# Kernel tuning notes

Measured on AMD Instinct MI355X. Metric: run time of the kernel, lower is better.

Reference implementation:

```python
import jax, jax.numpy as jnp
import numpy as np

B, T, M, PH, PW = 4, 8, 128, 48, 48
QD, CD, H, DH = 1024, 768, 8, 64
INNER = H * DH

def layer_norm(x, g, b, eps=1e-5):
    m = x.mean(-1, keepdims=True)
    v = ((x - m) ** 2).mean(-1, keepdims=True)
    return (x - m) * jax.lax.rsqrt(v + eps) * g + b

def setup_inputs():
    key = jax.random.key(0)
    ks = jax.random.split(key, 10)
    x = jax.random.normal(ks[0], (B * T, PH * PW, QD), jnp.float32)
    context = jax.random.normal(ks[1], (B, M, CD), jnp.float32)
    sg_node_positions = jax.random.normal(ks[2], (B, M, 3), jnp.float32) * 2.0
    # valid c2w: identity rotation + random translation (invertible)
    c2w = jnp.broadcast_to(jnp.eye(4, dtype=jnp.float32), (B, T, 4, 4))
    camera_c2w = c2w.at[..., :3, 3].set(jax.random.normal(ks[3], (B, T, 3), jnp.float32))
    intrinsics = jnp.broadcast_to(jnp.array([[1.0, 0.0, 0.5], [0.0, 1.0, 0.5], [0.0, 0.0, 1.0]], jnp.float32), (B, 3, 3))
    s = 0.02
    Wq = jax.random.normal(ks[4], (QD, INNER), jnp.float32) * s
    Wk = jax.random.normal(ks[5], (CD, INNER), jnp.float32) * s
    Wv = jax.random.normal(ks[6], (CD, INNER), jnp.float32) * s
    Wo = jax.random.normal(ks[7], (INNER, QD), jnp.float32) * s
    gate = jnp.array([0.1], jnp.float32)          # zero-init in module; nonzero so path is active
    spatial_gate = jnp.array([0.1], jnp.float32)
    spatial_log_sigma = jax.random.normal(ks[8], (H,), jnp.float32) * 0.1
    depth_log_alpha = jax.random.normal(ks[9], (H,), jnp.float32) * 0.1
    gamma_q = jnp.ones((QD,), jnp.float32); beta_q = jnp.zeros((QD,), jnp.float32)
    gamma_k = jnp.ones((CD,), jnp.float32); beta_k = jnp.zeros((CD,), jnp.float32)
    return dict(x=x, context=context, sg_node_positions=sg_node_positions, camera_c2w=camera_c2w,
                intrinsics=intrinsics, Wq=Wq, Wk=Wk, Wv=Wv, Wo=Wo, gate=gate, spatial_gate=spatial_gate,
                spatial_log_sigma=spatial_log_sigma, depth_log_alpha=depth_log_alpha,
                gamma_q=gamma_q, beta_q=beta_q, gamma_k=gamma_k, beta_k=beta_k,
                patch_h=PH, patch_w=PW)

def spatial_bias(sg_node_positions, camera_c2w, intrinsics, spatial_log_sigma, depth_log_alpha, patch_h, patch_w):
    Bb, Mn, _ = sg_node_positions.shape
    Tn = camera_c2w.shape[1]
    w2c = jnp.linalg.inv(camera_c2w)
    R = w2c[:, :, :3, :3]
    tv = w2c[:, :, :3, 3]
    p_cam = jnp.einsum('btij,bmj->btmi', R, sg_node_positions) + tv[:, :, None, :]  # (B,T,M,3)
    z = jnp.clip(p_cam[..., 2], 1e-4, None)
    fx = intrinsics[:, 0, 0]; fy = intrinsics[:, 1, 1]
    cx = intrinsics[:, 0, 2]; cy = intrinsics[:, 1, 2]
    u = fx[:, None, None] * (p_cam[..., 0] / z) + cx[:, None, None]   # (B,T,M)
    v = fy[:, None, None] * (p_cam[..., 1] / z) + cy[:, None, None]
    gy = (jnp.arange(patch_h, dtype=jnp.float32) + 0.5) / patch_h
    gx = (jnp.arange(patch_w, dtype=jnp.float32) + 0.5) / patch_w
    gyy, gxx = jnp.meshgrid(gy, gx, indexing='ij')
    gxx = gxx.reshape(-1); gyy = gyy.reshape(-1)                       # (P,)
    sq = (gxx[None, None, :, None] - u[:, :, None, :]) ** 2 + (gyy[None, None, :, None] - v[:, :, None, :]) ** 2  # (B,T,P,M)
    sigma = jnp.exp(spatial_log_sigma)
    inv2s = z[:, :, None, :] ** 2 / (2.0 * sigma[None, None, :, None] ** 2 + 1e-8)  # (B,T,H,M)
    bias = -sq[:, :, None, :, :] * inv2s[:, :, :, None, :]             # (B,T,H,P,M)
    depth_term = depth_log_alpha[None, None, :, None, None] * (-jnp.log(z))[:, :, None, None, :]
    bias = bias + depth_term
    behind = p_cam[..., 2] <= 0.0
    bias = jnp.where(behind[:, :, None, None, :], 0.0, bias)
    return bias.reshape(Bb * Tn, bias.shape[2], patch_h * patch_w, Mn)  # (BT,H,P,M)

def reference(x, context, sg_node_positions, camera_c2w, intrinsics, Wq, Wk, Wv, Wo, gate, spatial_gate,
              spatial_log_sigma, depth_log_alpha, gamma_q, beta_q, gamma_k, beta_k, patch_h, patch_w):
    BT, P, _ = x.shape
    Bb, Mn, _ = context.shape
    Tn = camera_c2w.shape[1]
    q = layer_norm(x, gamma_q, beta_q) @ Wq                            # (BT,P,INNER)
    ck = layer_norm(context, gamma_k, beta_k)
    k = ck @ Wk
    v = ck @ Wv
    q = q.reshape(BT, P, H, DH).transpose(0, 2, 1, 3)                  # (BT,H,P,DH)
    k = jnp.broadcast_to(k.reshape(Bb, 1, Mn, H, DH), (Bb, Tn, Mn, H, DH)).reshape(BT, Mn, H, DH).transpose(0, 2, 1, 3)
    v = jnp.broadcast_to(v.reshape(Bb, 1, Mn, H, DH), (Bb, Tn, Mn, H, DH)).reshape(BT, Mn, H, DH).transpose(0, 2, 1, 3)
    scores = jnp.einsum('bhpd,bhmd->bhpm', q, k) * (DH ** -0.5)        # (BT,H,P,M)
    bias = spatial_bias(sg_node_positions, camera_c2w, intrinsics, spatial_log_sigma, depth_log_alpha, patch_h, patch_w)
    scores = scores + jnp.tanh(spatial_gate) * bias
    attn = jax.nn.softmax(scores, axis=-1)
    out = jnp.einsum('bhpm,bhmd->bhpd', attn, v).transpose(0, 2, 1, 3).reshape(BT, P, INNER)
    return x + jnp.tanh(gate) * (out @ Wo)
```

## Files before the change

### kernel.cpp

```cpp
#include <hip/hip_runtime.h>
#include <hip/hip_bf16.h>
#include <stdint.h>
#include <cstddef>

typedef short short8 __attribute__((ext_vector_type(8)));
typedef float f32x4 __attribute__((ext_vector_type(4)));
typedef unsigned short us4 __attribute__((ext_vector_type(4)));

#define DEV static __device__ __forceinline__

DEV unsigned short f2b(float f) {
  __hip_bfloat16 h = __float2bfloat16(f);
  return __builtin_bit_cast(unsigned short, h);
}

DEV void gload_lds16(const void* g, void* lds) {
  __builtin_amdgcn_global_load_lds((const __attribute__((address_space(1))) unsigned int*)g,
                                   (__attribute__((address_space(3))) unsigned int*)lds, 16, 0, 0);
}

template<int EPI>
__launch_bounds__(256, 2)
__global__ void gemm_bt(const unsigned short* __restrict__ A,
                        const unsigned short* __restrict__ Bt,
                        unsigned short* __restrict__ Cb,
                        float* __restrict__ Cf,
                        const float* __restrict__ xres,
                        const float* __restrict__ gatep,
                        int M, int N, int K)
{
  __shared__ __attribute__((aligned(16))) char As[16384];
  __shared__ __attribute__((aligned(16))) char Bs[16384];
  const int tid  = threadIdx.x;
  const int lane = tid & 63, w = tid >> 6;
  const int wr = w >> 1, wc = w & 1;
  const int g = lane >> 4, lr = lane & 15;
  const int ntile = N >> 7;
  const int m0 = (blockIdx.x / ntile) << 7;
  const int n0 = (blockIdx.x % ntile) << 7;

  const int lrow  = lane >> 3;
  const int lslot = (lane & 7) ^ lrow;

  f32x4 acc[4][4] = {};

  for (int k0 = 0; k0 < K; k0 += 64) {
#pragma unroll
    for (int c = 0; c < 4; ++c) {
      const int rowc = (w*4 + c)*8;
      gload_lds16(A  + (size_t)(m0 + rowc + lrow)*K + k0 + lslot*8, As + rowc*128);
      gload_lds16(Bt + (size_t)(n0 + rowc + lrow)*K + k0 + lslot*8, Bs + rowc*128);
    }
    __syncthreads();
#pragma unroll
    for (int ks = 0; ks < 2; ++ks) {
      short8 af[4], bfr[4];
#pragma unroll
      for (int mt = 0; mt < 4; ++mt) {
        int row = wr*64 + mt*16 + lr;
        int slot = (ks*4 + g) ^ (row & 7);
        af[mt] = *(const short8*)(As + row*128 + slot*16);
      }
#pragma unroll
      for (int nt = 0; nt < 4; ++nt) {
        int row = wc*64 + nt*16 + lr;
        int slot = (ks*4 + g) ^ (row & 7);
        bfr[nt] = *(const short8*)(Bs + row*128 + slot*16);
      }
#pragma unroll
      for (int mt = 0; mt < 4; ++mt)
#pragma unroll
        for (int nt = 0; nt < 4; ++nt)
          acc[mt][nt] = __builtin_amdgcn_mfma_f32_16x16x32_bf16(af[mt], bfr[nt], acc[mt][nt], 0, 0, 0);
    }
    __syncthreads();
  }

  if (EPI == 1) {
    const float tg = tanhf(gatep[0]);
#pragma unroll
    for (int mt = 0; mt < 4; ++mt)
#pragma unroll
      for (int nt = 0; nt < 4; ++nt)
#pragma unroll
        for (int r = 0; r < 4; ++r) {
          size_t row = (size_t)(m0 + wr*64 + mt*16 + g*4 + r);
          size_t col = (size_t)(n0 + wc*64 + nt*16 + lr);
          size_t idx = row * (size_t)N + col;
          Cf[idx] = xres[idx] + tg * acc[mt][nt][r];
        }
  } else {
#pragma unroll
    for (int mt = 0; mt < 4; ++mt)
#pragma unroll
      for (int nt = 0; nt < 4; ++nt)
#pragma unroll
        for (int r = 0; r < 4; ++r) {
          size_t row = (size_t)(m0 + wr*64 + mt*16 + g*4 + r);
          size_t col = (size_t)(n0 + wc*64 + nt*16 + lr);
          Cb[row * (size_t)N + col] = f2b(acc[mt][nt][r]);
        }
  }
}

template<int NSEG>
__global__ void ln_rows(const float* __restrict__ in, const float* __restrict__ gamma,
                        const float* __restrict__ beta, unsigned short* __restrict__ out, int C)
{
  const int lane = threadIdx.x & 63;
  const size_t row = (size_t)blockIdx.x*4 + (threadIdx.x >> 6);
  const float* rp = in + row * (size_t)C;
  f32x4 vals[NSEG];
  float s = 0.f, sq = 0.f;
#pragma unroll
  for (int i = 0; i < NSEG; ++i) {
    f32x4 v = *(const f32x4*)(rp + (i*64 + lane)*4);
    vals[i] = v;
#pragma unroll
    for (int j = 0; j < 4; ++j) { s += v[j]; sq += v[j]*v[j]; }
  }
#pragma unroll
  for (int off = 32; off >= 1; off >>= 1) {
    s  += __shfl_xor(s, off);
    sq += __shfl_xor(sq, off);
  }
  const float invC = 1.0f / (float)C;
  float mean = s * invC;
  float var  = sq * invC - mean*mean;
  float rstd = rsqrtf(var + 1e-5f);
#pragma unroll
  for (int i = 0; i < NSEG; ++i) {
    int cb = (i*64 + lane)*4;
    f32x4 gm = *(const f32x4*)(gamma + cb);
    f32x4 bb = *(const f32x4*)(beta + cb);
    us4 ov;
#pragma unroll
    for (int j = 0; j < 4; ++j)
      ov[j] = f2b((vals[i][j] - mean)*rstd*gm[j] + bb[j]);
    *(us4*)(out + row * (size_t)C + cb) = ov;
  }
}

__global__ void transpose_cast(const float* __restrict__ src, unsigned short* __restrict__ dst,
                               int R, int C)
{
  __shared__ float tile[32][33];
  const int cb = C >> 5;
  const int bx = blockIdx.x % cb, by = blockIdx.x / cb;
  const int tx = threadIdx.x & 31, ty = threadIdx.x >> 5;
#pragma unroll
  for (int i = 0; i < 32; i += 8)
    tile[ty + i][tx] = src[(size_t)(by*32 + ty + i)*C + bx*32 + tx];
  __syncthreads();
#pragma unroll
  for (int i = 0; i < 32; i += 8)
    dst[(size_t)(bx*32 + ty + i)*R + by*32 + tx] = f2b(tile[tx][ty + i]);
}

__global__ void spatial_pre(const float* __restrict__ pos, const float* __restrict__ c2w,
                            const float* __restrict__ intr, const float* __restrict__ sls,
                            const float* __restrict__ dla,
                            float* __restrict__ u_o, float* __restrict__ v_o, float* __restrict__ bh_o,
                            float* __restrict__ iv_o, float* __restrict__ dp_o)
{
  const int bt = blockIdx.x;
  const int b = bt >> 3;
  const int m = threadIdx.x;
  const float* Mc = c2w + (size_t)bt*16;
  float r00=Mc[0], r01=Mc[1], r02=Mc[2],  t0=Mc[3];
  float r10=Mc[4], r11=Mc[5], r12=Mc[6],  t1=Mc[7];
  float r20=Mc[8], r21=Mc[9], r22=Mc[10], t2=Mc[11];
  float a00 = r11*r22 - r12*r21;
  float a01 = r02*r21 - r01*r22;
  float a02 = r01*r12 - r02*r11;
  float a10 = r12*r20 - r10*r22;
  float a11 = r00*r22 - r02*r20;
  float a12 = r02*r10 - r00*r12;
  float a20 = r10*r21 - r11*r20;
  float a21 = r01*r20 - r00*r21;
  float a22 = r00*r11 - r01*r10;
  float det = r00*a00 + r01*a10 + r02*a20;
  float id = 1.0f/det;
  a00*=id; a01*=id; a02*=id; a10*=id; a11*=id; a12*=id; a20*=id; a21*=id; a22*=id;
  float tv0 = -(a00*t0 + a01*t1 + a02*t2);
  float tv1 = -(a10*t0 + a11*t1 + a12*t2);
  float tv2 = -(a20*t0 + a21*t1 + a22*t2);
  const float* pm = pos + (size_t)(b*128 + m)*3;
  float px = pm[0], py = pm[1], pz = pm[2];
  float x = a00*px + a01*py + a02*pz + tv0;
  float y = a10*px + a11*py + a12*pz + tv1;
  float zraw = a20*px + a21*py + a22*pz + tv2;
  float z = fmaxf(zraw, 1e-4f);
  float fx = intr[b*9 + 0], fy = intr[b*9 + 4], cx = intr[b*9 + 2], cy = intr[b*9 + 5];
  u_o[bt*128 + m] = fx*(x/z) + cx;
  v_o[bt*128 + m] = fy*(y/z) + cy;
  bh_o[bt*128 + m] = (zraw <= 0.0f) ? 1.0f : 0.0f;
  float lz = __logf(z);
#pragma unroll
  for (int hh = 0; hh < 8; ++hh) {
    float sg = __expf(sls[hh]);
    iv_o[(size_t)(bt*8 + hh)*128 + m] = z*z / (2.0f*sg*sg + 1e-8f);
    dp_o[(size_t)(bt*8 + hh)*128 + m] = dla[hh] * (-lz);
  }
}

__global__ void reshuffle_kv(const unsigned short* __restrict__ kproj,
                             const unsigned short* __restrict__ vproj,
                             unsigned short* __restrict__ Kb, unsigned short* __restrict__ Vt)
{
  int idx = blockIdx.x*256 + threadIdx.x;
  int d  = idx & 63;
  int hh = (idx >> 6) & 7;
  int m  = (idx >> 9) & 127;
  int b  = idx >> 16;
  unsigned short kv = kproj[idx];
  unsigned short vv = vproj[idx];
  Kb[(((size_t)(b*8 + hh))*128 + m)*64 + d] = kv;
  Vt[(((size_t)(b*8 + hh))*64 + d)*128 + m] = vv;
}

__launch_bounds__(256, 2)
__global__ void attn_kernel(const unsigned short* __restrict__ q,
                            const unsigned short* __restrict__ Kb,
                            const unsigned short* __restrict__ Vt,
                            const float* __restrict__ ub, const float* __restrict__ vb,
                            const float* __restrict__ bhb,
                            const float* __restrict__ ivb, const float* __restrict__ dpb,
                            const float* __restrict__ sgate,
                            unsigned short* __restrict__ out)
{
  const int bid = blockIdx.x;
  const int ptile = bid % 18;
  const int h  = (bid / 18) & 7;
  const int bt = bid / (18*8);
  const int b  = bt >> 3;
  const int lane = threadIdx.x & 63, w = threadIdx.x >> 6;
  const int g = lane >> 4, lr = lane & 15;
  const int p0 = ptile*128 + w*32;

  const float sg = tanhf(sgate[0]);
  const unsigned short* Kh = Kb + ((size_t)(b*8 + h)) * (128*64);
  const unsigned short* Vh = Vt + ((size_t)(b*8 + h)) * (64*128);
  const unsigned short* qh = q + (size_t)bt*2304*512 + h*64;

  short8 qf[2][2];
#pragma unroll
  for (int pt = 0; pt < 2; ++pt)
#pragma unroll
    for (int ks = 0; ks < 2; ++ks)
      qf[pt][ks] = *(const short8*)(qh + (size_t)(p0 + pt*16 + lr)*512 + ks*32 + g*8);

  f32x4 st[8][2] = {};
#pragma unroll
  for (int mt = 0; mt < 8; ++mt) {
#pragma unroll
    for (int ks = 0; ks < 2; ++ks) {
      short8 kf = *(const short8*)(Kh + (mt*16 + lr)*64 + ks*32 + g*8);
#pragma unroll
      for (int pt = 0; pt < 2; ++pt)
        st[mt][pt] = __builtin_amdgcn_mfma_f32_16x16x32_bf16(kf, qf[pt][ks], st[mt][pt], 0, 0, 0);
    }
  }

  float gx[2], gy[2];
#pragma unroll
  for (int pt = 0; pt < 2; ++pt) {
    int p = p0 + pt*16 + lr;
    int py = p / 48, px = p - py*48;
    gx[pt] = (px + 0.5f) * (1.0f/48.0f);
    gy[pt] = (py + 0.5f) * (1.0f/48.0f);
  }
  const float* uB = ub  + bt*128;
  const float* vB = vb  + bt*128;
  const float* bB = bhb + bt*128;
  const float* iB = ivb + (size_t)(bt*8 + h)*128;
  const float* dB = dpb + (size_t)(bt*8 + h)*128;

  float pmax[2] = {-3.0e38f, -3.0e38f};
#pragma unroll
  for (int mt = 0; mt < 8; ++mt) {
    int mb = mt*16 + g*4;
    f32x4 uu = *(const f32x4*)(uB + mb);
    f32x4 vv = *(const f32x4*)(vB + mb);
    f32x4 bh = *(const f32x4*)(bB + mb);
    f32x4 iv = *(const f32x4*)(iB + mb);
    f32x4 dp = *(const f32x4*)(dB + mb);
#pragma unroll
    for (int r = 0; r < 4; ++r) {
#pragma unroll
      for (int pt = 0; pt < 2; ++pt) {
        float du = gx[pt] - uu[r], dv = gy[pt] - vv[r];
        float bias = (bh[r] != 0.0f) ? 0.0f : (-(du*du + dv*dv)*iv[r] + dp[r]);
        float s = st[mt][pt][r]*0.125f + sg*bias;
        st[mt][pt][r] = s;
        pmax[pt] = fmaxf(pmax[pt], s);
      }
    }
  }
#pragma unroll
  for (int pt = 0; pt < 2; ++pt) {
    pmax[pt] = fmaxf(pmax[pt], __shfl_xor(pmax[pt], 16));
    pmax[pt] = fmaxf(pmax[pt], __shfl_xor(pmax[pt], 32));
  }
  float psum[2] = {0.f, 0.f};
#pragma unroll
  for (int mt = 0; mt < 8; ++mt)
#pragma unroll
    for (int pt = 0; pt < 2; ++pt)
#pragma unroll
      for (int r = 0; r < 4; ++r) {
        float e = __expf(st[mt][pt][r] - pmax[pt]);
        st[mt][pt][r] = e;
        psum[pt] += e;
      }
#pragma unroll
  for (int pt = 0; pt < 2; ++pt) {
    psum[pt] += __shfl_xor(psum[pt], 16);
    psum[pt] += __shfl_xor(psum[pt], 32);
  }
  float pinv[2] = {1.0f/psum[0], 1.0f/psum[1]};

  short8 pf[2][4];
#pragma unroll
  for (int pt = 0; pt < 2; ++pt)
#pragma unroll
    for (int ms = 0; ms < 4; ++ms)
#pragma unroll
      for (int i = 0; i < 8; ++i)
        pf[pt][ms][i] = (short)f2b(st[ms*2 + (i>>2)][pt][i & 3] * pinv[pt]);

  f32x4 o[4][2] = {};
#pragma unroll
  for (int ms = 0; ms < 4; ++ms) {
#pragma unroll
    for (int dt = 0; dt < 4; ++dt) {
      const unsigned short* vp = Vh + (size_t)(dt*16 + lr)*128 + ms*32 + g*4;
      us4 v0 = *(const us4*)(vp);
      us4 v1 = *(const us4*)(vp + 16);
      short8 vf;
#pragma unroll
      for (int i = 0; i < 4; ++i) { vf[i] = (short)v0[i]; vf[i+4] = (short)v1[i]; }
#pragma unroll
      for (int pt = 0; pt < 2; ++pt)
        o[dt][pt] = __builtin_amdgcn_mfma_f32_16x16x32_bf16(vf, pf[pt][ms], o[dt][pt], 0, 0, 0);
    }
  }

#pragma unroll
  for (int dt = 0; dt < 4; ++dt)
#pragma unroll
    for (int pt = 0; pt < 2; ++pt) {
      int p = p0 + pt*16 + lr;
      int d = h*64 + dt*16 + g*4;
      us4 ov;
#pragma unroll
      for (int r = 0; r < 4; ++r) ov[r] = f2b(o[dt][pt][r]);
      *(us4*)(out + (size_t)(bt*2304 + p)*512 + d) = ov;
    }
}

extern "C" void kernel_launch(void* const* d_in, const int* in_sizes, int n_in,
                              void* d_out, int out_size, void* d_ws, size_t ws_size,
                              hipStream_t stream)
{
  const float* x     = (const float*)d_in[0];
  const float* ctx   = (const float*)d_in[1];
  const float* pos   = (const float*)d_in[2];
  const float* c2w   = (const float*)d_in[3];
  const float* intr  = (const float*)d_in[4];
  const float* Wq    = (const float*)d_in[5];
  const float* Wk    = (const float*)d_in[6];
  const float* Wv    = (const float*)d_in[7];
  const float* Wo    = (const float*)d_in[8];
  const float* gate  = (const float*)d_in[9];
  const float* sgate = (const float*)d_in[10];
  const float* sls   = (const float*)d_in[11];
  const float* dla   = (const float*)d_in[12];
  const float* gq    = (const float*)d_in[13];
  const float* bq    = (const float*)d_in[14];
  const float* gk    = (const float*)d_in[15];
  const float* bk    = (const float*)d_in[16];

  char* ws = (char*)d_ws;
  size_t off = 0;
  auto alloc = [&](size_t bytes) {
    char* p = ws + off;
    off += (bytes + 255) & ~(size_t)255;
    return p;
  };
  unsigned short* ln_x  = (unsigned short*)alloc(73728ull*1024*2);
  unsigned short* qbuf  = (unsigned short*)alloc(73728ull*512*2);
  unsigned short* Wq_t  = (unsigned short*)alloc(512ull*1024*2);
  unsigned short* Wk_t  = (unsigned short*)alloc(512ull*768*2);
  unsigned short* Wv_t  = (unsigned short*)alloc(512ull*768*2);
  unsigned short* Wo_t  = (unsigned short*)alloc(1024ull*512*2);
  unsigned short* ck    = (unsigned short*)alloc(512ull*768*2);
  unsigned short* kproj = (unsigned short*)alloc(512ull*512*2);
  unsigned short* vproj = (unsigned short*)alloc(512ull*512*2);
  unsigned short* Kbuf  = (unsigned short*)alloc(4ull*8*128*64*2);
  unsigned short* Vtb   = (unsigned short*)alloc(4ull*8*64*128*2);
  float* u_o  = (float*)alloc(32*128*4);
  float* v_o  = (float*)alloc(32*128*4);
  float* bh_o = (float*)alloc(32*128*4);
  float* iv_o = (float*)alloc(32ull*8*128*4);
  float* dp_o = (float*)alloc(32ull*8*128*4);
  unsigned short* attn_out = ln_x;

  transpose_cast<<<(512/32)*(1024/32), 256, 0, stream>>>(Wq, Wq_t, 1024, 512);
  transpose_cast<<<(512/32)*(768/32),  256, 0, stream>>>(Wk, Wk_t, 768, 512);
  transpose_cast<<<(512/32)*(768/32),  256, 0, stream>>>(Wv, Wv_t, 768, 512);
  transpose_cast<<<(1024/32)*(512/32), 256, 0, stream>>>(Wo, Wo_t, 512, 1024);

  ln_rows<4><<<73728/4, 256, 0, stream>>>(x, gq, bq, ln_x, 1024);
  ln_rows<3><<<512/4,   256, 0, stream>>>(ctx, gk, bk, ck, 768);

  spatial_pre<<<32, 128, 0, stream>>>(pos, c2w, intr, sls, dla, u_o, v_o, bh_o, iv_o, dp_o);

  gemm_bt<0><<<(512/128)*(512/128), 256, 0, stream>>>(ck, Wk_t, kproj, nullptr, nullptr, nullptr, 512, 512, 768);
  gemm_bt<0><<<(512/128)*(512/128), 256, 0, stream>>>(ck, Wv_t, vproj, nullptr, nullptr, nullptr, 512, 512, 768);
  reshuffle_kv<<<262144/256, 256, 0, stream>>>(kproj, vproj, Kbuf, Vtb);

  gemm_bt<0><<<(73728/128)*(512/128), 256, 0, stream>>>(ln_x, Wq_t, qbuf, nullptr, nullptr, nullptr, 73728, 512, 1024);

  attn_kernel<<<32*8*18, 256, 0, stream>>>(qbuf, Kbuf, Vtb, u_o, v_o, bh_o, iv_o, dp_o, sgate, attn_out);

  gemm_bt<1><<<(73728/128)*(1024/128), 256, 0, stream>>>(attn_out, Wo_t, nullptr, (float*)d_out, x, gate, 73728, 1024, 512);
}
```

Before: 559.8 us.

## Fuse attention with output projection and KV GEMMs with reshuffle

The attention kernel now handles all 8 heads for a 64-row patch tile, keeps the attention output in LDS, and runs the Wo projection plus the gated residual epilogue in the same kernel. This removes the bf16 attention-output round trip through global memory. The K/V projections are merged into one kernel that writes the head-major layout directly, which drops the reshuffle kernel, and the four weight transposes become one launch. In exchange, the fused kernel uses 80KB of LDS and launches only 1152 blocks, so occupancy drops, and each block reloads the full Wo matrix.

```diff
diff --git a/kernel.cpp b/kernel.cpp
--- a/kernel.cpp
+++ b/kernel.cpp
@@ -19,14 +19,10 @@
                                    (__attribute__((address_space(3))) unsigned int*)lds, 16, 0, 0);
 }
 
-template<int EPI>
 __launch_bounds__(256, 2)
 __global__ void gemm_bt(const unsigned short* __restrict__ A,
                         const unsigned short* __restrict__ Bt,
                         unsigned short* __restrict__ Cb,
-                        float* __restrict__ Cf,
-                        const float* __restrict__ xres,
-                        const float* __restrict__ gatep,
                         int M, int N, int K)
 {
   __shared__ __attribute__((aligned(16))) char As[16384];
@@ -76,31 +72,86 @@
     __syncthreads();
   }
 
-  if (EPI == 1) {
-    const float tg = tanhf(gatep[0]);
-#pragma unroll
-    for (int mt = 0; mt < 4; ++mt)
-#pragma unroll
-      for (int nt = 0; nt < 4; ++nt)
-#pragma unroll
-        for (int r = 0; r < 4; ++r) {
-          size_t row = (size_t)(m0 + wr*64 + mt*16 + g*4 + r);
-          size_t col = (size_t)(n0 + wc*64 + nt*16 + lr);
-          size_t idx = row * (size_t)N + col;
-          Cf[idx] = xres[idx] + tg * acc[mt][nt][r];
-        }
-  } else {
-#pragma unroll
-    for (int mt = 0; mt < 4; ++mt)
-#pragma unroll
-      for (int nt = 0; nt < 4; ++nt)
-#pragma unroll
-        for (int r = 0; r < 4; ++r) {
-          size_t row = (size_t)(m0 + wr*64 + mt*16 + g*4 + r);
-          size_t col = (size_t)(n0 + wc*64 + nt*16 + lr);
-          Cb[row * (size_t)N + col] = f2b(acc[mt][nt][r]);
-        }
-  }
+#pragma unroll
+  for (int mt = 0; mt < 4; ++mt)
+#pragma unroll
+    for (int nt = 0; nt < 4; ++nt)
+#pragma unroll
+      for (int r = 0; r < 4; ++r) {
+        size_t row = (size_t)(m0 + wr*64 + mt*16 + g*4 + r);
+        size_t col = (size_t)(n0 + wc*64 + nt*16 + lr);
+        Cb[row * (size_t)N + col] = f2b(acc[mt][nt][r]);
+      }
+}
+
+__launch_bounds__(256, 2)
+__global__ void gemm_kv(const unsigned short* __restrict__ ck,
+                        const unsigned short* __restrict__ Wk_t,
+                        const unsigned short* __restrict__ Wv_t,
+                        unsigned short* __restrict__ Kb,
+                        unsigned short* __restrict__ Vt)
+{
+  __shared__ __attribute__((aligned(16))) char As[16384];
+  __shared__ __attribute__((aligned(16))) char Bs[16384];
+  const int bid = blockIdx.x;
+  const int kv = bid >> 4, bidl = bid & 15;
+  const unsigned short* Bt = kv ? Wv_t : Wk_t;
+  const int m0 = (bidl >> 2) << 7, n0 = (bidl & 3) << 7;
+  const int tid  = threadIdx.x;
+  const int lane = tid & 63, w = tid >> 6;
+  const int wr = w >> 1, wc = w & 1;
+  const int g = lane >> 4, lr = lane & 15;
+  const int lrow  = lane >> 3;
+  const int lslot = (lane & 7) ^ lrow;
+  const int K = 768;
+
+  f32x4 acc[4][4] = {};
+
+  for (int k0 = 0; k0 < K; k0 += 64) {
+#pragma unroll
+    for (int c = 0; c < 4; ++c) {
+      const int rowc = (w*4 + c)*8;
+      gload_lds16(ck + (size_t)(m0 + rowc + lrow)*K + k0 + lslot*8, As + rowc*128);
+      gload_lds16(Bt + (size_t)(n0 + rowc + lrow)*K + k0 + lslot*8, Bs + rowc*128);
+    }
+    __syncthreads();
+#pragma unroll
+    for (int ks = 0; ks < 2; ++ks) {
+      short8 af[4], bfr[4];
+#pragma unroll
+      for (int mt = 0; mt < 4; ++mt) {
+        int row = wr*64 + mt*16 + lr;
+        int slot = (ks*4 + g) ^ (row & 7);
+        af[mt] = *(const short8*)(As + row*128 + slot*16);
+      }
+#pragma unroll
+      for (int nt = 0; nt < 4; ++nt) {
+        int row = wc*64 + nt*16 + lr;
+        int slot = (ks*4 + g) ^ (row & 7);
+        bfr[nt] = *(const short8*)(Bs + row*128 + slot*16);
+      }
+#pragma unroll
+      for (int mt = 0; mt < 4; ++mt)
+#pragma unroll
+        for (int nt = 0; nt < 4; ++nt)
+          acc[mt][nt] = __builtin_amdgcn_mfma_f32_16x16x32_bf16(af[mt], bfr[nt], acc[mt][nt], 0, 0, 0);
+    }
+    __syncthreads();
+  }
+
+#pragma unroll
+  for (int mt = 0; mt < 4; ++mt)
+#pragma unroll
+    for (int nt = 0; nt < 4; ++nt)
+#pragma unroll
+      for (int r = 0; r < 4; ++r) {
+        int row = m0 + wr*64 + mt*16 + g*4 + r;
+        int col = n0 + wc*64 + nt*16 + lr;
+        int bb = row >> 7, mm = row & 127, hh = col >> 6, dd = col & 63;
+        unsigned short val = f2b(acc[mt][nt][r]);
+        if (kv == 0) Kb[(((size_t)(bb*8 + hh))*128 + mm)*64 + dd] = val;
+        else         Vt[(((size_t)(bb*8 + hh))*64 + dd)*128 + mm] = val;
+      }
 }
 
 template<int NSEG>
@@ -141,12 +192,20 @@
   }
 }
 
-__global__ void transpose_cast(const float* __restrict__ src, unsigned short* __restrict__ dst,
-                               int R, int C)
+__global__ void transpose_all(const float* __restrict__ Wq, const float* __restrict__ Wk,
+                              const float* __restrict__ Wv, const float* __restrict__ Wo,
+                              unsigned short* __restrict__ Wq_t, unsigned short* __restrict__ Wk_t,
+                              unsigned short* __restrict__ Wv_t, unsigned short* __restrict__ Wo_t)
 {
   __shared__ float tile[32][33];
+  int bidx = blockIdx.x;
+  const float* src; unsigned short* dst; int R, C;
+  if (bidx < 512)       { src = Wq; dst = Wq_t; R = 1024; C = 512; }
+  else if (bidx < 896)  { src = Wk; dst = Wk_t; R = 768;  C = 512;  bidx -= 512; }
+  else if (bidx < 1280) { src = Wv; dst = Wv_t; R = 768;  C = 512;  bidx -= 896; }
+  else                  { src = Wo; dst = Wo_t; R = 512;  C = 1024; bidx -= 1280; }
   const int cb = C >> 5;
-  const int bx = blockIdx.x % cb, by = blockIdx.x / cb;
+  const int bx = bidx % cb, by = bidx / cb;
   const int tx = threadIdx.x & 31, ty = threadIdx.x >> 5;
 #pragma unroll
   for (int i = 0; i < 32; i += 8)
@@ -204,159 +263,189 @@
   }
 }
 
-__global__ void reshuffle_kv(const unsigned short* __restrict__ kproj,
-                             const unsigned short* __restrict__ vproj,
-                             unsigned short* __restrict__ Kb, unsigned short* __restrict__ Vt)
-{
-  int idx = blockIdx.x*256 + threadIdx.x;
-  int d  = idx & 63;
-  int hh = (idx >> 6) & 7;
-  int m  = (idx >> 9) & 127;
-  int b  = idx >> 16;
-  unsigned short kv = kproj[idx];
-  unsigned short vv = vproj[idx];
-  Kb[(((size_t)(b*8 + hh))*128 + m)*64 + d] = kv;
-  Vt[(((size_t)(b*8 + hh))*64 + d)*128 + m] = vv;
-}
-
 __launch_bounds__(256, 2)
-__global__ void attn_kernel(const unsigned short* __restrict__ q,
-                            const unsigned short* __restrict__ Kb,
-                            const unsigned short* __restrict__ Vt,
-                            const float* __restrict__ ub, const float* __restrict__ vb,
-                            const float* __restrict__ bhb,
-                            const float* __restrict__ ivb, const float* __restrict__ dpb,
-                            const float* __restrict__ sgate,
-                            unsigned short* __restrict__ out)
-{
+__global__ void attn_oproj(const unsigned short* __restrict__ q,
+                           const unsigned short* __restrict__ Kb,
+                           const unsigned short* __restrict__ Vt,
+                           const unsigned short* __restrict__ Wo_t,
+                           const float* __restrict__ ub, const float* __restrict__ vb,
+                           const float* __restrict__ bhb,
+                           const float* __restrict__ ivb, const float* __restrict__ dpb,
+                           const float* __restrict__ sgate, const float* __restrict__ gatep,
+                           const float* __restrict__ xres,
+                           float* __restrict__ outp)
+{
+  __shared__ __attribute__((aligned(16))) char oT[65536];
+  __shared__ __attribute__((aligned(16))) char WoS[16384];
+
   const int bid = blockIdx.x;
-  const int ptile = bid % 18;
-  const int h  = (bid / 18) & 7;
-  const int bt = bid / (18*8);
+  const int ptile = bid % 36;
+  const int bt = bid / 36;
   const int b  = bt >> 3;
   const int lane = threadIdx.x & 63, w = threadIdx.x >> 6;
   const int g = lane >> 4, lr = lane & 15;
-  const int p0 = ptile*128 + w*32;
-
+
+  const int prow_l = w*16 + lr;
+  const int p = ptile*64 + prow_l;
   const float sg = tanhf(sgate[0]);
-  const unsigned short* Kh = Kb + ((size_t)(b*8 + h)) * (128*64);
-  const unsigned short* Vh = Vt + ((size_t)(b*8 + h)) * (64*128);
-  const unsigned short* qh = q + (size_t)bt*2304*512 + h*64;
-
-  short8 qf[2][2];
-#pragma unroll
-  for (int pt = 0; pt < 2; ++pt)
-#pragma unroll
-    for (int ks = 0; ks < 2; ++ks)
-      qf[pt][ks] = *(const short8*)(qh + (size_t)(p0 + pt*16 + lr)*512 + ks*32 + g*8);
-
-  f32x4 st[8][2] = {};
-#pragma unroll
-  for (int mt = 0; mt < 8; ++mt) {
-#pragma unroll
-    for (int ks = 0; ks < 2; ++ks) {
-      short8 kf = *(const short8*)(Kh + (mt*16 + lr)*64 + ks*32 + g*8);
-#pragma unroll
-      for (int pt = 0; pt < 2; ++pt)
-        st[mt][pt] = __builtin_amdgcn_mfma_f32_16x16x32_bf16(kf, qf[pt][ks], st[mt][pt], 0, 0, 0);
-    }
-  }
-
-  float gx[2], gy[2];
-#pragma unroll
-  for (int pt = 0; pt < 2; ++pt) {
-    int p = p0 + pt*16 + lr;
-    int py = p / 48, px = p - py*48;
-    gx[pt] = (px + 0.5f) * (1.0f/48.0f);
-    gy[pt] = (py + 0.5f) * (1.0f/48.0f);
-  }
-  const float* uB = ub  + bt*128;
-  const float* vB = vb  + bt*128;
-  const float* bB = bhb + bt*128;
-  const float* iB = ivb + (size_t)(bt*8 + h)*128;
-  const float* dB = dpb + (size_t)(bt*8 + h)*128;
-
-  float pmax[2] = {-3.0e38f, -3.0e38f};
-#pragma unroll
-  for (int mt = 0; mt < 8; ++mt) {
-    int mb = mt*16 + g*4;
-    f32x4 uu = *(const f32x4*)(uB + mb);
-    f32x4 vv = *(const f32x4*)(vB + mb);
-    f32x4 bh = *(const f32x4*)(bB + mb);
-    f32x4 iv = *(const f32x4*)(iB + mb);
-    f32x4 dp = *(const f32x4*)(dB + mb);
-#pragma unroll
-    for (int r = 0; r < 4; ++r) {
-#pragma unroll
-      for (int pt = 0; pt < 2; ++pt) {
-        float du = gx[pt] - uu[r], dv = gy[pt] - vv[r];
-        float bias = (bh[r] != 0.0f) ? 0.0f : (-(du*du + dv*dv)*iv[r] + dp[r]);
-        float s = st[mt][pt][r]*0.125f + sg*bias;
-        st[mt][pt][r] = s;
-        pmax[pt] = fmaxf(pmax[pt], s);
-      }
-    }
-  }
-#pragma unroll
-  for (int pt = 0; pt < 2; ++pt) {
-    pmax[pt] = fmaxf(pmax[pt], __shfl_xor(pmax[pt], 16));
-    pmax[pt] = fmaxf(pmax[pt], __shfl_xor(pmax[pt], 32));
-  }
-  float psum[2] = {0.f, 0.f};
-#pragma unroll
-  for (int mt = 0; mt < 8; ++mt)
-#pragma unroll
-    for (int pt = 0; pt < 2; ++pt)
-#pragma unroll
-      for (int r = 0; r < 4; ++r) {
-        float e = __expf(st[mt][pt][r] - pmax[pt]);
-        st[mt][pt][r] = e;
-        psum[pt] += e;
-      }
-#pragma unroll
-  for (int pt = 0; pt < 2; ++pt) {
-    psum[pt] += __shfl_xor(psum[pt], 16);
-    psum[pt] += __shfl_xor(psum[pt], 32);
-  }
-  float pinv[2] = {1.0f/psum[0], 1.0f/psum[1]};
-
-  short8 pf[2][4];
-#pragma unroll
-  for (int pt = 0; pt < 2; ++pt)
-#pragma unroll
-    for (int ms = 0; ms < 4; ++ms)
-#pragma unroll
-      for (int i = 0; i < 8; ++i)
-        pf[pt][ms][i] = (short)f2b(st[ms*2 + (i>>2)][pt][i & 3] * pinv[pt]);
-
-  f32x4 o[4][2] = {};
-#pragma unroll
-  for (int ms = 0; ms < 4; ++ms) {
-#pragma unroll
-    for (int dt = 0; dt < 4; ++dt) {
-      const unsigned short* vp = Vh + (size_t)(dt*16 + lr)*128 + ms*32 + g*4;
-      us4 v0 = *(const us4*)(vp);
-      us4 v1 = *(const us4*)(vp + 16);
-      short8 vf;
-#pragma unroll
-      for (int i = 0; i < 4; ++i) { vf[i] = (short)v0[i]; vf[i+4] = (short)v1[i]; }
-#pragma unroll
-      for (int pt = 0; pt < 2; ++pt)
-        o[dt][pt] = __builtin_amdgcn_mfma_f32_16x16x32_bf16(vf, pf[pt][ms], o[dt][pt], 0, 0, 0);
-    }
-  }
-
-#pragma unroll
-  for (int dt = 0; dt < 4; ++dt)
-#pragma unroll
-    for (int pt = 0; pt < 2; ++pt) {
-      int p = p0 + pt*16 + lr;
-      int d = h*64 + dt*16 + g*4;
-      us4 ov;
-#pragma unroll
-      for (int r = 0; r < 4; ++r) ov[r] = f2b(o[dt][pt][r]);
-      *(us4*)(out + (size_t)(bt*2304 + p)*512 + d) = ov;
-    }
+  {
+    const int py = p / 48, px = p - py*48;
+    const float gx = (px + 0.5f) * (1.0f/48.0f);
+    const float gy = (py + 0.5f) * (1.0f/48.0f);
+    const float* uB = ub  + bt*128;
+    const float* vB = vb  + bt*128;
+    const float* bB = bhb + bt*128;
+
+    for (int h = 0; h < 8; ++h) {
+      const unsigned short* Kh = Kb + ((size_t)(b*8 + h)) * (128*64);
+      const unsigned short* Vh = Vt + ((size_t)(b*8 + h)) * (64*128);
+      const unsigned short* qh = q + ((size_t)(bt*2304 + p))*512 + h*64;
+      const float* iB = ivb + (size_t)(bt*8 + h)*128;
+      const float* dB = dpb + (size_t)(bt*8 + h)*128;
+
+      short8 qf[2];
+#pragma unroll
+      for (int ks = 0; ks < 2; ++ks)
+        qf[ks] = *(const short8*)(qh + ks*32 + g*8);
+
+      f32x4 st[8] = {};
+#pragma unroll
+      for (int mt = 0; mt < 8; ++mt) {
+#pragma unroll
+        for (int ks = 0; ks < 2; ++ks) {
+          short8 kf = *(const short8*)(Kh + (mt*16 + lr)*64 + ks*32 + g*8);
+          st[mt] = __builtin_amdgcn_mfma_f32_16x16x32_bf16(kf, qf[ks], st[mt], 0, 0, 0);
+        }
+      }
+
+      float pmax = -3.0e38f;
+#pragma unroll
+      for (int mt = 0; mt < 8; ++mt) {
+        int mb = mt*16 + g*4;
+        f32x4 uu = *(const f32x4*)(uB + mb);
+        f32x4 vv = *(const f32x4*)(vB + mb);
+        f32x4 bh = *(const f32x4*)(bB + mb);
+        f32x4 iv = *(const f32x4*)(iB + mb);
+        f32x4 dp = *(const f32x4*)(dB + mb);
+#pragma unroll
+        for (int r = 0; r < 4; ++r) {
+          float du = gx - uu[r], dv = gy - vv[r];
+          float bias = (bh[r] != 0.0f) ? 0.0f : (-(du*du + dv*dv)*iv[r] + dp[r]);
+          float s = st[mt][r]*0.125f + sg*bias;
+          st[mt][r] = s;
+          pmax = fmaxf(pmax, s);
+        }
+      }
+      pmax = fmaxf(pmax, __shfl_xor(pmax, 16));
+      pmax = fmaxf(pmax, __shfl_xor(pmax, 32));
+      float psum = 0.f;
+#pragma unroll
+      for (int mt = 0; mt < 8; ++mt)
+#pragma unroll
+        for (int r = 0; r < 4; ++r) {
+          float e = __expf(st[mt][r] - pmax);
+          st[mt][r] = e;
+          psum += e;
+        }
+      psum += __shfl_xor(psum, 16);
+      psum += __shfl_xor(psum, 32);
+      const float pinv = 1.0f/psum;
+
+      short8 pf[4];
+#pragma unroll
+      for (int ms = 0; ms < 4; ++ms)
+#pragma unroll
+        for (int i = 0; i < 8; ++i)
+          pf[ms][i] = (short)f2b(st[ms*2 + (i>>2)][i & 3] * pinv);
+
+      f32x4 o[4] = {};
+#pragma unroll
+      for (int ms = 0; ms < 4; ++ms) {
+#pragma unroll
+        for (int dt = 0; dt < 4; ++dt) {
+          const unsigned short* vp = Vh + (size_t)(dt*16 + lr)*128 + ms*32 + g*4;
+          us4 v0 = *(const us4*)(vp);
+          us4 v1 = *(const us4*)(vp + 16);
+          short8 vf;
+#pragma unroll
+          for (int i = 0; i < 4; ++i) { vf[i] = (short)v0[i]; vf[i+4] = (short)v1[i]; }
+          o[dt] = __builtin_amdgcn_mfma_f32_16x16x32_bf16(vf, pf[ms], o[dt], 0, 0, 0);
+        }
+      }
+
+#pragma unroll
+      for (int dt = 0; dt < 4; ++dt) {
+        int d = h*64 + dt*16 + g*4;
+        us4 ov;
+#pragma unroll
+        for (int r = 0; r < 4; ++r) ov[r] = f2b(o[dt][r]);
+        int slot = (d >> 3) ^ (prow_l & 7);
+        *(us4*)(oT + prow_l*1024 + slot*16 + (d & 7)*2) = ov;
+      }
+    }
+  }
+  __syncthreads();
+
+  const int wm = w >> 1, wn = w & 1;
+  const int lrow  = lane >> 3;
+  const int lslot = (lane & 7) ^ lrow;
+  const float tg = tanhf(gatep[0]);
+  float* Sw = (float*)(WoS) + w*1024;
+
+  for (int nb = 0; nb < 8; ++nb) {
+    f32x4 acc[2][4] = {};
+    for (int k0 = 0; k0 < 512; k0 += 64) {
+#pragma unroll
+      for (int c = 0; c < 4; ++c) {
+        const int rowc = (w*4 + c)*8;
+        gload_lds16(Wo_t + (size_t)(nb*128 + rowc + lrow)*512 + k0 + lslot*8, WoS + rowc*128);
+      }
+      __syncthreads();
+#pragma unroll
+      for (int ks = 0; ks < 2; ++ks) {
+        short8 af[2], bfr[4];
+#pragma unroll
+        for (int mt = 0; mt < 2; ++mt) {
+          int row = wm*32 + mt*16 + lr;
+          int sgl = (k0 >> 3) + ks*4 + g;
+          af[mt] = *(const short8*)(oT + row*1024 + ((sgl ^ (row & 7))*16));
+        }
+#pragma unroll
+        for (int nt = 0; nt < 4; ++nt) {
+          int row = wn*64 + nt*16 + lr;
+          int slot = (ks*4 + g) ^ (row & 7);
+          bfr[nt] = *(const short8*)(WoS + row*128 + slot*16);
+        }
+#pragma unroll
+        for (int mt = 0; mt < 2; ++mt)
+#pragma unroll
+          for (int nt = 0; nt < 4; ++nt)
+            acc[mt][nt] = __builtin_amdgcn_mfma_f32_16x16x32_bf16(af[mt], bfr[nt], acc[mt][nt], 0, 0, 0);
+      }
+      __syncthreads();
+    }
+#pragma unroll
+    for (int mt = 0; mt < 2; ++mt) {
+#pragma unroll
+      for (int nt = 0; nt < 4; ++nt)
+#pragma unroll
+        for (int r = 0; r < 4; ++r)
+          Sw[(g*4 + r)*64 + nt*16 + lr] = acc[mt][nt][r];
+#pragma unroll
+      for (int rep = 0; rep < 4; ++rep) {
+        int row2 = rep*4 + g;
+        int lcol = lr*4;
+        f32x4 val = *(const f32x4*)(Sw + row2*64 + lcol);
+        size_t rowg = (size_t)(bt*2304 + ptile*64 + wm*32 + mt*16 + row2);
+        size_t colg = (size_t)(nb*128 + wn*64 + lcol);
+        size_t idx = rowg*1024 + colg;
+        f32x4 xv = *(const f32x4*)(xres + idx);
+#pragma unroll
+        for (int j = 0; j < 4; ++j) val[j] = xv[j] + tg*val[j];
+        *(f32x4*)(outp + idx) = val;
+      }
+    }
+  }
 }
 
 extern "C" void kernel_launch(void* const* d_in, const int* in_sizes, int n_in,
@@ -395,8 +484,6 @@
   unsigned short* Wv_t  = (unsigned short*)alloc(512ull*768*2);
   unsigned short* Wo_t  = (unsigned short*)alloc(1024ull*512*2);
   unsigned short* ck    = (unsigned short*)alloc(512ull*768*2);
-  unsigned short* kproj = (unsigned short*)alloc(512ull*512*2);
-  unsigned short* vproj = (unsigned short*)alloc(512ull*512*2);
   unsigned short* Kbuf  = (unsigned short*)alloc(4ull*8*128*64*2);
   unsigned short* Vtb   = (unsigned short*)alloc(4ull*8*64*128*2);
   float* u_o  = (float*)alloc(32*128*4);
@@ -404,25 +491,19 @@
   float* bh_o = (float*)alloc(32*128*4);
   float* iv_o = (float*)alloc(32ull*8*128*4);
   float* dp_o = (float*)alloc(32ull*8*128*4);
-  unsigned short* attn_out = ln_x;
-
-  transpose_cast<<<(512/32)*(1024/32), 256, 0, stream>>>(Wq, Wq_t, 1024, 512);
-  transpose_cast<<<(512/32)*(768/32),  256, 0, stream>>>(Wk, Wk_t, 768, 512);
-  transpose_cast<<<(512/32)*(768/32),  256, 0, stream>>>(Wv, Wv_t, 768, 512);
-  transpose_cast<<<(1024/32)*(512/32), 256, 0, stream>>>(Wo, Wo_t, 512, 1024);
+
+  transpose_all<<<1792, 256, 0, stream>>>(Wq, Wk, Wv, Wo, Wq_t, Wk_t, Wv_t, Wo_t);
 
   ln_rows<4><<<73728/4, 256, 0, stream>>>(x, gq, bq, ln_x, 1024);
   ln_rows<3><<<512/4,   256, 0, stream>>>(ctx, gk, bk, ck, 768);
 
   spatial_pre<<<32, 128, 0, stream>>>(pos, c2w, intr, sls, dla, u_o, v_o, bh_o, iv_o, dp_o);
 
-  gemm_bt<0><<<(512/128)*(512/128), 256, 0, stream>>>(ck, Wk_t, kproj, nullptr, nullptr, nullptr, 512, 512, 768);
-  gemm_bt<0><<<(512/128)*(512/128), 256, 0, stream>>>(ck, Wv_t, vproj, nullptr, nullptr, nullptr, 512, 512, 768);
-  reshuffle_kv<<<262144/256, 256, 0, stream>>>(kproj, vproj, Kbuf, Vtb);
-
-  gemm_bt<0><<<(73728/128)*(512/128), 256, 0, stream>>>(ln_x, Wq_t, qbuf, nullptr, nullptr, nullptr, 73728, 512, 1024);
-
-  attn_kernel<<<32*8*18, 256, 0, stream>>>(qbuf, Kbuf, Vtb, u_o, v_o, bh_o, iv_o, dp_o, sgate, attn_out);
-
-  gemm_bt<1><<<(73728/128)*(1024/128), 256, 0, stream>>>(attn_out, Wo_t, nullptr, (float*)d_out, x, gate, 73728, 1024, 512);
-}
+  gemm_kv<<<32, 256, 0, stream>>>(ck, Wk_t, Wv_t, Kbuf, Vtb);
+
+  gemm_bt<<<(73728/128)*(512/128), 256, 0, stream>>>(ln_x, Wq_t, qbuf, 73728, 512, 1024);
+
+  attn_oproj<<<32*36, 256, 0, stream>>>(qbuf, Kbuf, Vtb, Wo_t,
+                                        u_o, v_o, bh_o, iv_o, dp_o,
+                                        sgate, gate, x, (float*)d_out);
+}
```

Measured after the change: 764.1 us. 36.5% more time.

## Stage GEMM epilogues through LDS, swizzle tile order, fuse KV GEMMs and transposes

Applied to the files above, without the earlier changes.

The GEMM epilogue now stages accumulators through LDS so the residual/gate and bf16 stores go out as wide, row-contiguous vector accesses instead of scattered scalar stores. Block indices are remapped in groups of 8 to change the tile order across the grid for cache locality. The K and V projection GEMMs are merged into one launch that writes straight into the attention layouts, which removes the reshuffle kernel. The four weight-transpose launches are merged into one. The LDS staging reuses the A buffer after the main loop, so it relies on the final barrier and adds extra shared-memory traffic.

```diff
diff --git a/kernel.cpp b/kernel.cpp
--- a/kernel.cpp
+++ b/kernel.cpp
@@ -6,6 +6,7 @@
 typedef short short8 __attribute__((ext_vector_type(8)));
 typedef float f32x4 __attribute__((ext_vector_type(4)));
 typedef unsigned short us4 __attribute__((ext_vector_type(4)));
+typedef unsigned short us8 __attribute__((ext_vector_type(8)));
 
 #define DEV static __device__ __forceinline__
 
@@ -36,8 +37,11 @@
   const int wr = w >> 1, wc = w & 1;
   const int g = lane >> 4, lr = lane & 15;
   const int ntile = N >> 7;
-  const int m0 = (blockIdx.x / ntile) << 7;
-  const int n0 = (blockIdx.x % ntile) << 7;
+  const int nwg = gridDim.x;
+  const int bid = blockIdx.x;
+  const int tile = ((nwg & 7) == 0) ? ((bid & 7)*(nwg >> 3) + (bid >> 3)) : bid;
+  const int m0 = (tile / ntile) << 7;
+  const int n0 = (tile % ntile) << 7;
 
   const int lrow  = lane >> 3;
   const int lslot = (lane & 7) ^ lrow;
@@ -76,31 +80,121 @@
     __syncthreads();
   }
 
+  float* Sw = (float*)(As) + w*1024;
   if (EPI == 1) {
     const float tg = tanhf(gatep[0]);
 #pragma unroll
-    for (int mt = 0; mt < 4; ++mt)
+    for (int mt = 0; mt < 4; ++mt) {
 #pragma unroll
       for (int nt = 0; nt < 4; ++nt)
 #pragma unroll
-        for (int r = 0; r < 4; ++r) {
-          size_t row = (size_t)(m0 + wr*64 + mt*16 + g*4 + r);
-          size_t col = (size_t)(n0 + wc*64 + nt*16 + lr);
-          size_t idx = row * (size_t)N + col;
-          Cf[idx] = xres[idx] + tg * acc[mt][nt][r];
-        }
+        for (int r = 0; r < 4; ++r)
+          Sw[(g*4 + r)*64 + nt*16 + lr] = acc[mt][nt][r];
+#pragma unroll
+      for (int rep = 0; rep < 4; ++rep) {
+        int row2 = rep*4 + g;
+        int colf = lr*4;
+        f32x4 val = *(const f32x4*)(Sw + row2*64 + colf);
+        size_t rowg = (size_t)(m0 + wr*64 + mt*16 + row2);
+        size_t idx = rowg * (size_t)N + (n0 + wc*64 + colf);
+        f32x4 xv = *(const f32x4*)(xres + idx);
+#pragma unroll
+        for (int j = 0; j < 4; ++j) val[j] = xv[j] + tg*val[j];
+        *(f32x4*)(Cf + idx) = val;
+      }
+    }
   } else {
 #pragma unroll
-    for (int mt = 0; mt < 4; ++mt)
+    for (int mt = 0; mt < 4; ++mt) {
 #pragma unroll
       for (int nt = 0; nt < 4; ++nt)
 #pragma unroll
-        for (int r = 0; r < 4; ++r) {
-          size_t row = (size_t)(m0 + wr*64 + mt*16 + g*4 + r);
-          size_t col = (size_t)(n0 + wc*64 + nt*16 + lr);
-          Cb[row * (size_t)N + col] = f2b(acc[mt][nt][r]);
-        }
-  }
+        for (int r = 0; r < 4; ++r)
+          Sw[(g*4 + r)*64 + nt*16 + lr] = acc[mt][nt][r];
+#pragma unroll
+      for (int rep = 0; rep < 2; ++rep) {
+        int row2 = rep*8 + (lane >> 3);
+        int colf = (lane & 7)*8;
+        f32x4 a0 = *(const f32x4*)(Sw + row2*64 + colf);
+        f32x4 a1 = *(const f32x4*)(Sw + row2*64 + colf + 4);
+        us8 ov;
+#pragma unroll
+        for (int j = 0; j < 4; ++j) { ov[j] = f2b(a0[j]); ov[4+j] = f2b(a1[j]); }
+        size_t rowg = (size_t)(m0 + wr*64 + mt*16 + row2);
+        *(us8*)(Cb + rowg * (size_t)N + (n0 + wc*64 + colf)) = ov;
+      }
+    }
+  }
+}
+
+__launch_bounds__(256, 2)
+__global__ void gemm_kv(const unsigned short* __restrict__ ck,
+                        const unsigned short* __restrict__ Wk_t,
+                        const unsigned short* __restrict__ Wv_t,
+                        unsigned short* __restrict__ Kb,
+                        unsigned short* __restrict__ Vt)
+{
+  __shared__ __attribute__((aligned(16))) char As[16384];
+  __shared__ __attribute__((aligned(16))) char Bs[16384];
+  const int bid = blockIdx.x;
+  const int kv = bid >> 4, bidl = bid & 15;
+  const unsigned short* Bt = kv ? Wv_t : Wk_t;
+  const int m0 = (bidl >> 2) << 7, n0 = (bidl & 3) << 7;
+  const int tid  = threadIdx.x;
+  const int lane = tid & 63, w = tid >> 6;
+  const int wr = w >> 1, wc = w & 1;
+  const int g = lane >> 4, lr = lane & 15;
+  const int lrow  = lane >> 3;
+  const int lslot = (lane & 7) ^ lrow;
+  const int K = 768;
+
+  f32x4 acc[4][4] = {};
+
+  for (int k0 = 0; k0 < K; k0 += 64) {
+#pragma unroll
+    for (int c = 0; c < 4; ++c) {
+      const int rowc = (w*4 + c)*8;
+      gload_lds16(ck + (size_t)(m0 + rowc + lrow)*K + k0 + lslot*8, As + rowc*128);
+      gload_lds16(Bt + (size_t)(n0 + rowc + lrow)*K + k0 + lslot*8, Bs + rowc*128);
+    }
+    __syncthreads();
+#pragma unroll
+    for (int ks = 0; ks < 2; ++ks) {
+      short8 af[4], bfr[4];
+#pragma unroll
+      for (int mt = 0; mt < 4; ++mt) {
+        int row = wr*64 + mt*16 + lr;
+        int slot = (ks*4 + g) ^ (row & 7);
+        af[mt] = *(const short8*)(As + row*128 + slot*16);
+      }
+#pragma unroll
+      for (int nt = 0; nt < 4; ++nt) {
+        int row = wc*64 + nt*16 + lr;
+        int slot = (ks*4 + g) ^ (row & 7);
+        bfr[nt] = *(const short8*)(Bs + row*128 + slot*16);
+      }
+#pragma unroll
+      for (int mt = 0; mt < 4; ++mt)
+#pragma unroll
+        for (int nt = 0; nt < 4; ++nt)
+          acc[mt][nt] = __builtin_amdgcn_mfma_f32_16x16x32_bf16(af[mt], bfr[nt], acc[mt][nt], 0, 0, 0);
+    }
+    __syncthreads();
+  }
+
+#pragma unroll
+  for (int mt = 0; mt < 4; ++mt)
+#pragma unroll
+    for (int nt = 0; nt < 4; ++nt)
+#pragma unroll
+      for (int r = 0; r < 4; ++r) {
+        int row = m0 + wr*64 + mt*16 + g*4 + r;
+        int col = n0 + wc*64 + nt*16 + lr;
+        int bb = row >> 7, mm = row & 127, hh = col >> 6, dd = col & 63;
+        unsigned short val = f2b(acc[mt][nt][r]);
+        if (kv == 0) Kb[(((size_t)(bb*8 + hh))*128 + mm)*64 + dd] = val;
+        else         Vt[(((size_t)(bb*8 + hh))*64 + dd)*128 + mm] = val;
+      }
 }
 
 template<int NSEG>
@@ -141,12 +235,20 @@
   }
 }
 
-__global__ void transpose_cast(const float* __restrict__ src, unsigned short* __restrict__ dst,
-                               int R, int C)
+__global__ void transpose_all(const float* __restrict__ Wq, const float* __restrict__ Wk,
+                              const float* __restrict__ Wv, const float* __restrict__ Wo,
+                              unsigned short* __restrict__ Wq_t, unsigned short* __restrict__ Wk_t,
+                              unsigned short* __restrict__ Wv_t, unsigned short* __restrict__ Wo_t)
 {
   __shared__ float tile[32][33];
+  int bidx = blockIdx.x;
+  const float* src; unsigned short* dst; int R, C;
+  if (bidx < 512)       { src = Wq; dst = Wq_t; R = 1024; C = 512; }
+  else if (bidx < 896)  { src = Wk; dst = Wk_t; R = 768;  C = 512;  bidx -= 512; }
+  else if (bidx < 1280) { src = Wv; dst = Wv_t; R = 768;  C = 512;  bidx -= 896; }
+  else                  { src = Wo; dst = Wo_t; R = 512;  C = 1024; bidx -= 1280; }
   const int cb = C >> 5;
-  const int bx = blockIdx.x % cb, by = blockIdx.x / cb;
+  const int bx = bidx % cb, by = bidx / cb;
   const int tx = threadIdx.x & 31, ty = threadIdx.x >> 5;
 #pragma unroll
   for (int i = 0; i < 32; i += 8)
@@ -204,21 +306,6 @@
   }
 }
 
-__global__ void reshuffle_kv(const unsigned short* __restrict__ kproj,
-                             const unsigned short* __restrict__ vproj,
-                             unsigned short* __restrict__ Kb, unsigned short* __restrict__ Vt)
-{
-  int idx = blockIdx.x*256 + threadIdx.x;
-  int d  = idx & 63;
-  int hh = (idx >> 6) & 7;
-  int m  = (idx >> 9) & 127;
-  int b  = idx >> 16;
-  unsigned short kv = kproj[idx];
-  unsigned short vv = vproj[idx];
-  Kb[(((size_t)(b*8 + hh))*128 + m)*64 + d] = kv;
-  Vt[(((size_t)(b*8 + hh))*64 + d)*128 + m] = vv;
-}
-
 __launch_bounds__(256, 2)
 __global__ void attn_kernel(const unsigned short* __restrict__ q,
                             const unsigned short* __restrict__ Kb,
@@ -395,8 +482,6 @@
   unsigned short* Wv_t  = (unsigned short*)alloc(512ull*768*2);
   unsigned short* Wo_t  = (unsigned short*)alloc(1024ull*512*2);
   unsigned short* ck    = (unsigned short*)alloc(512ull*768*2);
-  unsigned short* kproj = (unsigned short*)alloc(512ull*512*2);
-  unsigned short* vproj = (unsigned short*)alloc(512ull*512*2);
   unsigned short* Kbuf  = (unsigned short*)alloc(4ull*8*128*64*2);
   unsigned short* Vtb   = (unsigned short*)alloc(4ull*8*64*128*2);
   float* u_o  = (float*)alloc(32*128*4);
@@ -406,19 +491,14 @@
   float* dp_o = (float*)alloc(32ull*8*128*4);
   unsigned short* attn_out = ln_x;
 
-  transpose_cast<<<(512/32)*(1024/32), 256, 0, stream>>>(Wq, Wq_t, 1024, 512);
-  transpose_cast<<<(512/32)*(768/32),  256, 0, stream>>>(Wk, Wk_t, 768, 512);
-  transpose_cast<<<(512/32)*(768/32),  256, 0, stream>>>(Wv, Wv_t, 768, 512);
-  transpose_cast<<<(1024/32)*(512/32), 256, 0, stream>>>(Wo, Wo_t, 512, 1024);
+  transpose_all<<<1792, 256, 0, stream>>>(Wq, Wk, Wv, Wo, Wq_t, Wk_t, Wv_t, Wo_t);
 
   ln_rows<4><<<73728/4, 256, 0, stream>>>(x, gq, bq, ln_x, 1024);
   ln_rows<3><<<512/4,   256, 0, stream>>>(ctx, gk, bk, ck, 768);
 
   spatial_pre<<<32, 128, 0, stream>>>(pos, c2w, intr, sls, dla, u_o, v_o, bh_o, iv_o, dp_o);
 
-  gemm_bt<0><<<(512/128)*(512/128), 256, 0, stream>>>(ck, Wk_t, kproj, nullptr, nullptr, nullptr, 512, 512, 768);
-  gemm_bt<0><<<(512/128)*(512/128), 256, 0, stream>>>(ck, Wv_t, vproj, nullptr, nullptr, nullptr, 512, 512, 768);
-  reshuffle_kv<<<262144/256, 256, 0, stream>>>(kproj, vproj, Kbuf, Vtb);
+  gemm_kv<<<32, 256, 0, stream>>>(ck, Wk_t, Wv_t, Kbuf, Vtb);
 
   gemm_bt<0><<<(73728/128)*(512/128), 256, 0, stream>>>(ln_x, Wq_t, qbuf, nullptr, nullptr, nullptr, 73728, 512, 1024);
 
```

Measured after the change: 506.7 us. 9.5% less time.
